# Optimization experiments

Hardware: AMD Instinct MI355X
Metric: run time of the kernel (lower is better)

The kernel has to match this reference:

```python
import jax, jax.numpy as jnp
import numpy as np

N_HIT = 50000
N_TRUE = 512
N_EDGE = 40000
D = 8
S_B = 1.0
Q_MIN = 0.5


def setup_inputs() -> dict:
    key = jax.random.key(0)
    k_x, k_f, k_y, k_eh, k_ep = jax.random.split(key, 5)
    x = jax.random.normal(k_x, (N_HIT, D), dtype=jnp.float32)
    # f is a sigmoid-like filter output in (0,1); keep away from 1 so atanh is finite
    f = jax.random.uniform(k_f, (N_HIT,), dtype=jnp.float32, minval=0.01, maxval=0.95)
    # y == -1 marks background hits; otherwise an instance id
    y = jax.random.randint(k_y, (N_HIT,), -1, N_TRUE, dtype=jnp.int64)
    e_h = jax.random.randint(k_eh, (N_EDGE,), 0, N_HIT, dtype=jnp.int64)
    e_p = jax.random.randint(k_ep, (N_EDGE,), 0, N_TRUE, dtype=jnp.int64)
    # guarantee every true particle has at least one assigned hit
    e_p = e_p.at[:N_TRUE].set(jnp.arange(N_TRUE, dtype=jnp.int64))
    return {"x": x, "f": f, "y": y, "e_h": e_h, "e_p": e_p}


def reference(x, f, y, e_h, e_p):
    n_hit = x.shape[0]
    fe = f[e_h]  # [n_edge]
    # scatter_max with zero-initialized output: clamp below at 0
    f_centers = jax.ops.segment_max(fe, e_p, num_segments=N_TRUE)
    f_centers = jnp.maximum(f_centers, 0.0)  # [n_true]
    # argmax hit per particle: among edges attaining the segment max, take largest hit id
    is_max = fe == f_centers[e_p]
    centers = jax.ops.segment_max(jnp.where(is_max, e_h, -1), e_p, num_segments=N_TRUE)  # [n_true]

    bkg_mask = y == -1
    n_bkg = bkg_mask.sum().astype(f.dtype)

    b1 = 1.0 - f_centers.sum() / N_TRUE
    b2 = S_B / n_bkg * jnp.where(bkg_mask, f, 0.0).sum()

    q = jnp.square(jnp.arctanh(f)) + Q_MIN  # [n_hit]

    # membership mask m_ik [n_hit, n_true]
    m_ik = jnp.zeros((n_hit, N_TRUE), dtype=bool).at[e_h, e_p].set(True)

    # pairwise squared distances to condensation centers [n_hit, n_true]
    xc = x[centers]  # [n_true, d]
    dist = jnp.sum(jnp.square(x[:, None, :] - xc[None, :, :]), axis=2)

    # attractive inside instance, hinged repulsive outside
    v = jnp.where(m_ik, dist, jnp.clip(1.0 - dist, 0.0))
    v = (jnp.sum(v * q[centers][None, :], axis=1) * q).sum() / n_hit

    return jnp.stack([b1 + b2, v])
```

## Files before the change

kernel.cpp:

```cpp
#include <hip/hip_runtime.h>
#include <math.h>

#define N_HIT  50000
#define N_TRUE 512
#define N_EDGE 40000
#define Q_MIN  0.5f

#define W_SEG     0
#define W_DONE    1024
#define W_VPART   1040
#define W_BKGF    1200
#define W_BKGN    1456
#define W_HREC    2048

#define K1_GRID   256
#define KSPLIT    32
#define KCH       (N_TRUE / KSPLIT)
#define HPT       13
#define HCHUNK    (256 * HPT)
#define NHB       ((N_HIT + HCHUNK - 1) / HCHUNK)
#define G2        (NHB * KSPLIT)
#define EPB2      79

__global__ __launch_bounds__(256) void k1(const float* __restrict__ x,
                                          const float* __restrict__ f,
                                          const int* __restrict__ y,
                                          const int* __restrict__ e_h,
                                          const int* __restrict__ e_p,
                                          unsigned* __restrict__ ws) {
    const int t = threadIdx.x, b = blockIdx.x;
    const int g = b * 256 + t;
    unsigned long long* __restrict__ seg = (unsigned long long*)ws;
    float2* __restrict__ hrec = (float2*)(ws + W_HREC);

    if (b == 0 && t < 9) {
        const int slot[9] = {W_DONE, W_VPART, W_VPART + 16, W_VPART + 32,
                             W_VPART + 48, W_VPART + 64, W_VPART + 80,
                             W_VPART + 96, W_VPART + 112};
        ws[slot[t]] = 0u;
    }

    if (g < N_EDGE) {
        const int h = e_h[g], p = e_p[g];
        const unsigned long long packed = 0x8000000000000000ull |
            ((unsigned long long)__float_as_uint(f[h]) << 32) | (unsigned)h;
        atomicMax(&seg[p], packed);
    }

    float sf = 0.f;
    bool isb = false;
    if (g < N_HIT) {
        const float4* xp = (const float4*)(x + (size_t)g * 8);
        const float4 x0 = xp[0], x1 = xp[1];
        float xi2 = x0.x * x0.x;
        xi2 = fmaf(x0.y, x0.y, xi2); xi2 = fmaf(x0.z, x0.z, xi2);
        xi2 = fmaf(x0.w, x0.w, xi2); xi2 = fmaf(x1.x, x1.x, xi2);
        xi2 = fmaf(x1.y, x1.y, xi2); xi2 = fmaf(x1.z, x1.z, xi2);
        xi2 = fmaf(x1.w, x1.w, xi2);
        const float fi = f[g];
        const float a  = atanhf(fi);
        hrec[g] = make_float2(xi2, fmaf(a, a, Q_MIN));
        isb = (y[g] == -1);
        if (isb) sf = fi;
    }
    for (int off = 32; off; off >>= 1) sf += __shfl_down(sf, off, 64);
    const unsigned long long bal = __ballot(isb);
    __shared__ float r[8];
    if ((t & 63) == 0) { r[t >> 6] = sf; r[4 + (t >> 6)] = (float)__popcll(bal); }
    __syncthreads();
    if (t == 0) {
        ((float*)ws)[W_BKGF + b] = r[0] + r[1] + r[2] + r[3];
        ((float*)ws)[W_BKGN + b] = r[4] + r[5] + r[6] + r[7];
    }
}

__global__ __launch_bounds__(256, 2) void k2(const float* __restrict__ x,
                                             const int* __restrict__ e_h,
                                             const int* __restrict__ e_p,
                                             unsigned* __restrict__ ws,
                                             float* __restrict__ out) {
    const int t = threadIdx.x, b = blockIdx.x;
    const unsigned long long* __restrict__ seg = (const unsigned long long*)ws;
    const float2* __restrict__ hrec = (const float2*)(ws + W_HREC);
    const int kb = b & (KSPLIT - 1);
    const int hb = b >> 5;

    __shared__ float ct[KCH * 12];
    __shared__ float r[4];
    if (t < KCH) {
        const unsigned long long w = seg[kb * KCH + t];
        const int c = (int)(unsigned)w;
        const float4* xp = (const float4*)(x + (size_t)c * 8);
        const float4 x0 = xp[0], x1 = xp[1];
        const float2 hc = hrec[c];
        *(float4*)(ct + 12 * t)     = make_float4(2.f * x0.x, 2.f * x0.y,
                                                  2.f * x0.z, 2.f * x0.w);
        *(float4*)(ct + 12 * t + 4) = make_float4(2.f * x1.x, 2.f * x1.y,
                                                  2.f * x1.z, 2.f * x1.w);
        ct[12 * t + 8] = 1.f - hc.x;
        ct[12 * t + 9] = hc.y;
    }
    __syncthreads();

    float4 xr0[HPT], xr1[HPT];
    float  xi2v[HPT], qiv[HPT], acc[HPT];
#pragma unroll
    for (int j = 0; j < HPT; ++j) {
        const int i = hb * HCHUNK + j * 256 + t;
        const bool valid = (i < N_HIT);
        const int  ic = valid ? i : 0;
        const float4* xp = (const float4*)(x + (size_t)ic * 8);
        xr0[j] = xp[0]; xr1[j] = xp[1];
        const float2 hq = hrec[ic];
        xi2v[j] = hq.x;
        qiv[j]  = valid ? hq.y : 0.f;
        acc[j]  = 0.f;
    }
#pragma unroll
    for (int k2i = 0; k2i < KCH; ++k2i) {
        const float4 c0  = *(const float4*)(ct + 12 * k2i);
        const float4 c1  = *(const float4*)(ct + 12 * k2i + 4);
        const float  tk  = ct[12 * k2i + 8];
        const float  qck = ct[12 * k2i + 9];
#pragma unroll
        for (int j = 0; j < HPT; ++j) {
            float s = tk - xi2v[j];
            s = fmaf(xr0[j].x, c0.x, s); s = fmaf(xr0[j].y, c0.y, s);
            s = fmaf(xr0[j].z, c0.z, s); s = fmaf(xr0[j].w, c0.w, s);
            s = fmaf(xr1[j].x, c1.x, s); s = fmaf(xr1[j].y, c1.y, s);
            s = fmaf(xr1[j].z, c1.z, s); s = fmaf(xr1[j].w, c1.w, s);
            const float rep = fmaxf(s, 0.f);
            acc[j] = fmaf(rep, qck, acc[j]);
        }
    }
    float vout = 0.f;
#pragma unroll
    for (int j = 0; j < HPT; ++j) vout = fmaf(acc[j], qiv[j], vout);

    if (t < EPB2) {
        const int e = b * EPB2 + t;
        if (e < N_EDGE) {
            const int h = e_h[e], p = e_p[e];
            const int c = (int)(unsigned)seg[p];
            const float4* hp4 = (const float4*)(x + (size_t)h * 8);
            const float4 a0 = hp4[0], a1 = hp4[1];
            const float4* cp4 = (const float4*)(x + (size_t)c * 8);
            const float4 c0 = cp4[0], c1 = cp4[1];
            const float2 hh = hrec[h], hc = hrec[c];
            float dot = a0.x * c0.x;
            dot = fmaf(a0.y, c0.y, dot); dot = fmaf(a0.z, c0.z, dot);
            dot = fmaf(a0.w, c0.w, dot); dot = fmaf(a1.x, c1.x, dot);
            dot = fmaf(a1.y, c1.y, dot); dot = fmaf(a1.z, c1.z, dot);
            dot = fmaf(a1.w, c1.w, dot);
            const float dist  = fmaf(-2.f, dot, hh.x + hc.x);
            const float hinge = fmaxf(1.f - dist, 0.f);
            vout = fmaf(hh.y * hc.y, dist - hinge, vout);
        }
    }

    for (int off = 32; off; off >>= 1) vout += __shfl_down(vout, off, 64);
    if ((t & 63) == 0) r[t >> 6] = vout;
    __syncthreads();

    __shared__ int last;
    if (t == 0) {
        atomicAdd((float*)ws + W_VPART + (b & 7) * 16, r[0] + r[1] + r[2] + r[3]);
        __threadfence();
        last = (atomicAdd(&ws[W_DONE], 1u) == G2 - 1);
    }
    __syncthreads();
    if (!last) return;
    __threadfence();

    float lfc = __uint_as_float((unsigned)(__hip_atomic_load(&seg[t], __ATOMIC_RELAXED,
                  __HIP_MEMORY_SCOPE_AGENT) >> 32) & 0x7FFFFFFFu)
              + __uint_as_float((unsigned)(__hip_atomic_load(&seg[t + 256], __ATOMIC_RELAXED,
                  __HIP_MEMORY_SCOPE_AGENT) >> 32) & 0x7FFFFFFFu);
    float lbf = __hip_atomic_load((const float*)ws + W_BKGF + t, __ATOMIC_RELAXED,
                                  __HIP_MEMORY_SCOPE_AGENT);
    float lbn = __hip_atomic_load((const float*)ws + W_BKGN + t, __ATOMIC_RELAXED,
                                  __HIP_MEMORY_SCOPE_AGENT);
    for (int off = 32; off; off >>= 1) {
        lfc += __shfl_down(lfc, off, 64);
        lbf += __shfl_down(lbf, off, 64);
        lbn += __shfl_down(lbn, off, 64);
    }
    __shared__ float fr[12];
    if ((t & 63) == 0) {
        fr[t >> 6] = lfc; fr[4 + (t >> 6)] = lbf; fr[8 + (t >> 6)] = lbn;
    }
    __syncthreads();
    if (t == 0) {
        float vs = 0.f;
        for (int s = 0; s < 8; ++s)
            vs += __hip_atomic_load((const float*)ws + W_VPART + s * 16,
                                    __ATOMIC_RELAXED, __HIP_MEMORY_SCOPE_AGENT);
        const float sum_fc  = fr[0] + fr[1] + fr[2] + fr[3];
        const float sum_bkg = fr[4] + fr[5] + fr[6] + fr[7];
        const float nb      = fr[8] + fr[9] + fr[10] + fr[11];
        out[0] = (1.f - sum_fc / (float)N_TRUE) + sum_bkg / nb;
        out[1] = vs / (float)N_HIT;
    }
}

extern "C" void kernel_launch(void* const* d_in, const int* in_sizes, int n_in,
                              void* d_out, int out_size, void* d_ws, size_t ws_size,
                              hipStream_t stream) {
    const float* x   = (const float*)d_in[0];
    const float* f   = (const float*)d_in[1];
    const int*   y   = (const int*)d_in[2];
    const int*   e_h = (const int*)d_in[3];
    const int*   e_p = (const int*)d_in[4];
    float* out = (float*)d_out;
    unsigned* ws = (unsigned*)d_ws;

    k1<<<K1_GRID, 256, 0, stream>>>(x, f, y, e_h, e_p, ws);
    k2<<<G2, 256, 0, stream>>>(x, e_h, e_p, ws, out);
}
```

Measured before the change: 93.41 us.

## Drop x-norm precompute from k1, recompute norms in k2, spread k1 work

```diff
diff --git a/kernel.cpp b/kernel.cpp
--- a/kernel.cpp
+++ b/kernel.cpp
@@ -9,68 +9,65 @@
 #define W_SEG     0
 #define W_DONE    1024
 #define W_VPART   1040
-#define W_BKGF    1200
-#define W_BKGN    1456
-#define W_HREC    2048
-
-#define K1_GRID   256
+#define W_BKGF    2048
+#define W_BKGN    2560
+#define W_QARR    4096
+
+#define K1_GRID   512
 #define KSPLIT    32
 #define KCH       (N_TRUE / KSPLIT)
 #define HPT       13
 #define HCHUNK    (256 * HPT)
-#define NHB       ((N_HIT + HCHUNK - 1) / HCHUNK)
+#define NHB       16
 #define G2        (NHB * KSPLIT)
-#define EPB2      79
-
-__global__ __launch_bounds__(256) void k1(const float* __restrict__ x,
-                                          const float* __restrict__ f,
+#define HPB       98
+#define EPB       79
+
+#define AG_LDF(p) __hip_atomic_load((p), __ATOMIC_RELAXED, __HIP_MEMORY_SCOPE_AGENT)
+
+__global__ __launch_bounds__(256) void k1(const float* __restrict__ f,
                                           const int* __restrict__ y,
                                           const int* __restrict__ e_h,
                                           const int* __restrict__ e_p,
                                           unsigned* __restrict__ ws) {
     const int t = threadIdx.x, b = blockIdx.x;
-    const int g = b * 256 + t;
     unsigned long long* __restrict__ seg = (unsigned long long*)ws;
-    float2* __restrict__ hrec = (float2*)(ws + W_HREC);
-
+    float* __restrict__ wsf = (float*)ws;
+
+    float sf = 0.f;
+    bool isb = false;
+    if (t < HPB) {
+        const int i = b * HPB + t;
+        if (i < N_HIT) {
+            const float fi = f[i];
+            const float a  = atanhf(fi);
+            wsf[W_QARR + i] = fmaf(a, a, Q_MIN);
+            isb = (y[i] == -1);
+            if (isb) sf = fi;
+        }
+    } else if (t >= 128 && t < 128 + EPB) {
+        const int e = b * EPB + (t - 128);
+        if (e < N_EDGE) {
+            const int h = e_h[e], p = e_p[e];
+            const unsigned long long packed = 0x8000000000000000ull |
+                ((unsigned long long)__float_as_uint(f[h]) << 32) | (unsigned)h;
+            atomicMax(&seg[p], packed);
+        }
+    }
+    for (int off = 32; off; off >>= 1) sf += __shfl_down(sf, off, 64);
+    const unsigned long long bal = __ballot(isb);
+    __shared__ float r[8];
+    if ((t & 63) == 0) { r[t >> 6] = sf; r[4 + (t >> 6)] = (float)__popcll(bal); }
+    __syncthreads();
+    if (t == 0) {
+        wsf[W_BKGF + b] = r[0] + r[1] + r[2] + r[3];
+        wsf[W_BKGN + b] = r[4] + r[5] + r[6] + r[7];
+    }
     if (b == 0 && t < 9) {
         const int slot[9] = {W_DONE, W_VPART, W_VPART + 16, W_VPART + 32,
                              W_VPART + 48, W_VPART + 64, W_VPART + 80,
                              W_VPART + 96, W_VPART + 112};
         ws[slot[t]] = 0u;
-    }
-
-    if (g < N_EDGE) {
-        const int h = e_h[g], p = e_p[g];
-        const unsigned long long packed = 0x8000000000000000ull |
-            ((unsigned long long)__float_as_uint(f[h]) << 32) | (unsigned)h;
-        atomicMax(&seg[p], packed);
-    }
-
-    float sf = 0.f;
-    bool isb = false;
-    if (g < N_HIT) {
-        const float4* xp = (const float4*)(x + (size_t)g * 8);
-        const float4 x0 = xp[0], x1 = xp[1];
-        float xi2 = x0.x * x0.x;
-        xi2 = fmaf(x0.y, x0.y, xi2); xi2 = fmaf(x0.z, x0.z, xi2);
-        xi2 = fmaf(x0.w, x0.w, xi2); xi2 = fmaf(x1.x, x1.x, xi2);
-        xi2 = fmaf(x1.y, x1.y, xi2); xi2 = fmaf(x1.z, x1.z, xi2);
-        xi2 = fmaf(x1.w, x1.w, xi2);
-        const float fi = f[g];
-        const float a  = atanhf(fi);
-        hrec[g] = make_float2(xi2, fmaf(a, a, Q_MIN));
-        isb = (y[g] == -1);
-        if (isb) sf = fi;
-    }
-    for (int off = 32; off; off >>= 1) sf += __shfl_down(sf, off, 64);
-    const unsigned long long bal = __ballot(isb);
-    __shared__ float r[8];
-    if ((t & 63) == 0) { r[t >> 6] = sf; r[4 + (t >> 6)] = (float)__popcll(bal); }
-    __syncthreads();
-    if (t == 0) {
-        ((float*)ws)[W_BKGF + b] = r[0] + r[1] + r[2] + r[3];
-        ((float*)ws)[W_BKGN + b] = r[4] + r[5] + r[6] + r[7];
     }
 }
 
@@ -81,7 +78,7 @@
                                              float* __restrict__ out) {
     const int t = threadIdx.x, b = blockIdx.x;
     const unsigned long long* __restrict__ seg = (const unsigned long long*)ws;
-    const float2* __restrict__ hrec = (const float2*)(ws + W_HREC);
+    const float* __restrict__ wsf = (const float*)ws;
     const int kb = b & (KSPLIT - 1);
     const int hb = b >> 5;
 
@@ -92,15 +89,18 @@
         const int c = (int)(unsigned)w;
         const float4* xp = (const float4*)(x + (size_t)c * 8);
         const float4 x0 = xp[0], x1 = xp[1];
-        const float2 hc = hrec[c];
+        float c2 = x0.x * x0.x;
+        c2 = fmaf(x0.y, x0.y, c2); c2 = fmaf(x0.z, x0.z, c2);
+        c2 = fmaf(x0.w, x0.w, c2); c2 = fmaf(x1.x, x1.x, c2);
+        c2 = fmaf(x1.y, x1.y, c2); c2 = fmaf(x1.z, x1.z, c2);
+        c2 = fmaf(x1.w, x1.w, c2);
         *(float4*)(ct + 12 * t)     = make_float4(2.f * x0.x, 2.f * x0.y,
                                                   2.f * x0.z, 2.f * x0.w);
         *(float4*)(ct + 12 * t + 4) = make_float4(2.f * x1.x, 2.f * x1.y,
                                                   2.f * x1.z, 2.f * x1.w);
-        ct[12 * t + 8] = 1.f - hc.x;
-        ct[12 * t + 9] = hc.y;
-    }
-    __syncthreads();
+        ct[12 * t + 8] = 1.f - c2;
+        ct[12 * t + 9] = wsf[W_QARR + c];
+    }
 
     float4 xr0[HPT], xr1[HPT];
     float  xi2v[HPT], qiv[HPT], acc[HPT];
@@ -111,11 +111,17 @@
         const int  ic = valid ? i : 0;
         const float4* xp = (const float4*)(x + (size_t)ic * 8);
         xr0[j] = xp[0]; xr1[j] = xp[1];
-        const float2 hq = hrec[ic];
-        xi2v[j] = hq.x;
-        qiv[j]  = valid ? hq.y : 0.f;
+        float s = xr0[j].x * xr0[j].x;
+        s = fmaf(xr0[j].y, xr0[j].y, s); s = fmaf(xr0[j].z, xr0[j].z, s);
+        s = fmaf(xr0[j].w, xr0[j].w, s); s = fmaf(xr1[j].x, xr1[j].x, s);
+        s = fmaf(xr1[j].y, xr1[j].y, s); s = fmaf(xr1[j].z, xr1[j].z, s);
+        s = fmaf(xr1[j].w, xr1[j].w, s);
+        xi2v[j] = s;
+        qiv[j]  = valid ? wsf[W_QARR + i] : 0.f;
         acc[j]  = 0.f;
     }
+    __syncthreads();
+
 #pragma unroll
     for (int k2i = 0; k2i < KCH; ++k2i) {
         const float4 c0  = *(const float4*)(ct + 12 * k2i);
@@ -137,8 +143,8 @@
 #pragma unroll
     for (int j = 0; j < HPT; ++j) vout = fmaf(acc[j], qiv[j], vout);
 
-    if (t < EPB2) {
-        const int e = b * EPB2 + t;
+    if (t < EPB) {
+        const int e = b * EPB + t;
         if (e < N_EDGE) {
             const int h = e_h[e], p = e_p[e];
             const int c = (int)(unsigned)seg[p];
@@ -146,15 +152,19 @@
             const float4 a0 = hp4[0], a1 = hp4[1];
             const float4* cp4 = (const float4*)(x + (size_t)c * 8);
             const float4 c0 = cp4[0], c1 = cp4[1];
-            const float2 hh = hrec[h], hc = hrec[c];
-            float dot = a0.x * c0.x;
-            dot = fmaf(a0.y, c0.y, dot); dot = fmaf(a0.z, c0.z, dot);
-            dot = fmaf(a0.w, c0.w, dot); dot = fmaf(a1.x, c1.x, dot);
-            dot = fmaf(a1.y, c1.y, dot); dot = fmaf(a1.z, c1.z, dot);
-            dot = fmaf(a1.w, c1.w, dot);
-            const float dist  = fmaf(-2.f, dot, hh.x + hc.x);
+            float dot = a0.x * c0.x, xh2 = a0.x * a0.x, xc2 = c0.x * c0.x;
+            dot = fmaf(a0.y, c0.y, dot); xh2 = fmaf(a0.y, a0.y, xh2); xc2 = fmaf(c0.y, c0.y, xc2);
+            dot = fmaf(a0.z, c0.z, dot); xh2 = fmaf(a0.z, a0.z, xh2); xc2 = fmaf(c0.z, c0.z, xc2);
+            dot = fmaf(a0.w, c0.w, dot); xh2 = fmaf(a0.w, a0.w, xh2); xc2 = fmaf(c0.w, c0.w, xc2);
+            dot = fmaf(a1.x, c1.x, dot); xh2 = fmaf(a1.x, a1.x, xh2); xc2 = fmaf(c1.x, c1.x, xc2);
+            dot = fmaf(a1.y, c1.y, dot); xh2 = fmaf(a1.y, a1.y, xh2); xc2 = fmaf(c1.y, c1.y, xc2);
+            dot = fmaf(a1.z, c1.z, dot); xh2 = fmaf(a1.z, a1.z, xh2); xc2 = fmaf(c1.z, c1.z, xc2);
+            dot = fmaf(a1.w, c1.w, dot); xh2 = fmaf(a1.w, a1.w, xh2); xc2 = fmaf(c1.w, c1.w, xc2);
+            const float dist  = fmaf(-2.f, dot, xh2 + xc2);
             const float hinge = fmaxf(1.f - dist, 0.f);
-            vout = fmaf(hh.y * hc.y, dist - hinge, vout);
+            const float qh = wsf[W_QARR + h];
+            const float qc = wsf[W_QARR + c];
+            vout = fmaf(qh * qc, dist - hinge, vout);
         }
     }
 
@@ -164,7 +174,7 @@
 
     __shared__ int last;
     if (t == 0) {
-        atomicAdd((float*)ws + W_VPART + (b & 7) * 16, r[0] + r[1] + r[2] + r[3]);
+        atomicAdd((float*)wsf + W_VPART + (b & 7) * 16, r[0] + r[1] + r[2] + r[3]);
         __threadfence();
         last = (atomicAdd(&ws[W_DONE], 1u) == G2 - 1);
     }
@@ -176,10 +186,8 @@
                   __HIP_MEMORY_SCOPE_AGENT) >> 32) & 0x7FFFFFFFu)
               + __uint_as_float((unsigned)(__hip_atomic_load(&seg[t + 256], __ATOMIC_RELAXED,
                   __HIP_MEMORY_SCOPE_AGENT) >> 32) & 0x7FFFFFFFu);
-    float lbf = __hip_atomic_load((const float*)ws + W_BKGF + t, __ATOMIC_RELAXED,
-                                  __HIP_MEMORY_SCOPE_AGENT);
-    float lbn = __hip_atomic_load((const float*)ws + W_BKGN + t, __ATOMIC_RELAXED,
-                                  __HIP_MEMORY_SCOPE_AGENT);
+    float lbf = AG_LDF(wsf + W_BKGF + t) + AG_LDF(wsf + W_BKGF + t + 256);
+    float lbn = AG_LDF(wsf + W_BKGN + t) + AG_LDF(wsf + W_BKGN + t + 256);
     for (int off = 32; off; off >>= 1) {
         lfc += __shfl_down(lfc, off, 64);
         lbf += __shfl_down(lbf, off, 64);
@@ -193,8 +201,7 @@
     if (t == 0) {
         float vs = 0.f;
         for (int s = 0; s < 8; ++s)
-            vs += __hip_atomic_load((const float*)ws + W_VPART + s * 16,
-                                    __ATOMIC_RELAXED, __HIP_MEMORY_SCOPE_AGENT);
+            vs += AG_LDF(wsf + W_VPART + s * 16);
         const float sum_fc  = fr[0] + fr[1] + fr[2] + fr[3];
         const float sum_bkg = fr[4] + fr[5] + fr[6] + fr[7];
         const float nb      = fr[8] + fr[9] + fr[10] + fr[11];
@@ -214,6 +221,6 @@
     float* out = (float*)d_out;
     unsigned* ws = (unsigned*)d_ws;
 
-    k1<<<K1_GRID, 256, 0, stream>>>(x, f, y, e_h, e_p, ws);
+    k1<<<K1_GRID, 256, 0, stream>>>(f, y, e_h, e_p, ws);
     k2<<<G2, 256, 0, stream>>>(x, e_h, e_p, ws, out);
 }
```

Result: faster. 89.78 us, median of 2 (-3.9%).
